# Kernel optimization log

Hardware: AMD Instinct MI355X
Metric: run time of the kernel (lower is better)

Reference implementation:

```python
import jax, jax.numpy as jnp
import numpy as np

NEG_INF = -1e30  # large negative in place of -inf for masked scores (fp32-safe)


def setup_inputs() -> dict:
    key = jax.random.key(0)
    kq, kk, kv, km = jax.random.split(key, 4)
    B, H, S, D = 2, 16, 2048, 64
    query = jax.random.normal(kq, (B, H, S, D), dtype=jnp.float32)
    k = jax.random.normal(kk, (B, H, S, D), dtype=jnp.float32)
    v = jax.random.normal(kv, (B, H, S, D), dtype=jnp.float32)
    mask = jax.random.randint(km, (B, H, S, S), 0, 2, dtype=jnp.int32)
    return {"query": query, "key": k, "value": v, "mask": mask}


def reference(query, key, value, mask):
    # Online-softmax chunked attention is mathematically exact softmax attention;
    # we compute the equivalent masked softmax attention in one fused expression.
    d_k = query.shape[-1]
    scale = 1.0 / np.sqrt(d_k).astype(np.float32)
    # scores: [B, H, Sq, Sk]
    scores = jnp.einsum('bhqd,bhkd->bhqk', query, key) * scale
    scores = jnp.where(mask == 0, NEG_INF, scores)
    attn = jax.nn.softmax(scores, axis=-1)
    out = jnp.einsum('bhqk,bhkd->bhqd', attn, value)
    return out
```

## Files before the change

kernel.cpp:

```cpp
#include <hip/hip_runtime.h>


typedef __attribute__((ext_vector_type(8))) short bf16x8;
typedef __attribute__((ext_vector_type(4))) short s16x4;
typedef __attribute__((ext_vector_type(4))) float f32x4;

#define S_LEN 2048
#define NT 32
#define PP 72
#define QSCALE 0.1803368801f

__device__ __forceinline__ short f2bf(float f) {
    union { float f; unsigned u; } v; v.f = f;
    unsigned r = v.u + 0x7fffu + ((v.u >> 16) & 1u);
    return (short)(r >> 16);
}

__device__ __forceinline__ float fexp2(float x) {
#if __has_builtin(__builtin_amdgcn_exp2f)
    return __builtin_amdgcn_exp2f(x);
#else
    return exp2f(x);
#endif
}

__device__ __forceinline__ bf16x8 cvt8(float4 a, float4 b, float s) {
    bf16x8 f;
    f[0]=f2bf(a.x*s); f[1]=f2bf(a.y*s); f[2]=f2bf(a.z*s); f[3]=f2bf(a.w*s);
    f[4]=f2bf(b.x*s); f[5]=f2bf(b.y*s); f[6]=f2bf(b.z*s); f[7]=f2bf(b.w*s);
    return f;
}

__global__ __launch_bounds__(256)
void pack_all(const float* __restrict__ Q, const float* __restrict__ K,
              const float* __restrict__ V, short* __restrict__ Qw,
              short* __restrict__ Kw, short* __restrict__ Vw) {
    __shared__ float vt[64][65];
    const int bh = blockIdx.x, t = blockIdx.y, which = blockIdx.z;
    if (which == 0) {
        for (int ci = threadIdx.x; ci < 512; ci += 256) {
            int ww = ci >> 7, ks = (ci >> 6) & 1, lane = ci & 63;
            int quad = lane >> 4, c = lane & 15;
            int row = t * 64 + ww * 16 + c;
            int d0 = ks * 32 + quad * 8;
            const float* src = Q + ((size_t)(bh * S_LEN + row)) * 64 + d0;
            float4 a = *(const float4*)src;
            float4 b = *(const float4*)(src + 4);
            *(bf16x8*)(Qw + ((size_t)(bh * 32 + t) * 512 + ci) * 8) = cvt8(a, b, QSCALE);
        }
    } else if (which == 1) {
        for (int ci = threadIdx.x; ci < 512; ci += 256) {
            int fb = ci >> 6, lane = ci & 63;
            int nb = fb >> 1, ks = fb & 1;
            int quad = lane >> 4, c = lane & 15;
            int key = t * 64 + c * 4 + nb;
            int d0 = ks * 32 + quad * 8;
            const float* src = K + ((size_t)(bh * S_LEN + key)) * 64 + d0;
            float4 a = *(const float4*)src;
            float4 b = *(const float4*)(src + 4);
            *(bf16x8*)(Kw + ((size_t)(bh * 32 + t) * 512 + ci) * 8) = cvt8(a, b, 1.0f);
        }
    } else {
        {
            int key = threadIdx.x >> 2, d0 = (threadIdx.x & 3) * 16;
            const float* src = V + ((size_t)(bh * S_LEN + t * 64 + key)) * 64 + d0;
            float4 a = *(const float4*)src;
            float4 b = *(const float4*)(src + 4);
            float4 cc = *(const float4*)(src + 8);
            float4 d = *(const float4*)(src + 12);
            float* dst = &vt[key][d0];
            dst[0]=a.x; dst[1]=a.y; dst[2]=a.z; dst[3]=a.w;
            dst[4]=b.x; dst[5]=b.y; dst[6]=b.z; dst[7]=b.w;
            dst[8]=cc.x; dst[9]=cc.y; dst[10]=cc.z; dst[11]=cc.w;
            dst[12]=d.x; dst[13]=d.y; dst[14]=d.z; dst[15]=d.w;
        }
        __syncthreads();
        for (int ci = threadIdx.x; ci < 512; ci += 256) {
            int fb = ci >> 6, lane = ci & 63;
            int db = fb >> 1, ks = fb & 1;
            int quad = lane >> 4, c = lane & 15;
            bf16x8 f;
#pragma unroll
            for (int j = 0; j < 8; ++j) {
                int pos = ks * 32 + quad * 8 + j;
                f[j] = f2bf(vt[pos][db * 16 + c]);
            }
            *(bf16x8*)(Vw + ((size_t)(bh * 32 + t) * 512 + ci) * 8) = f;
        }
    }
}

typedef __attribute__((address_space(3))) unsigned lds_u32;
typedef const __attribute__((address_space(1))) unsigned glob_u32;

__global__ __launch_bounds__(256, 3)
void fa_main(const short* __restrict__ Qw, const short* __restrict__ Kw,
             const short* __restrict__ Vw, const int* __restrict__ M,
             float* __restrict__ O) {
    __shared__ __align__(16) short Kb[2 * 8 * 512];
    __shared__ __align__(16) short Vb[2 * 8 * 512];
    __shared__ __align__(16) short Pwv[4 * 16 * PP];

    const int tid  = threadIdx.x;
    const int lane = tid & 63;
    const int w    = tid >> 6;
    const int quad = lane >> 4;
    const int c    = lane & 15;

    const int bid = blockIdx.x;
    const int x = bid & 7, y = bid >> 3;
    const int bh = x * 4 + (y >> 5);
    const int qt = y & 31;

    const short* qbase = Qw + ((size_t)(bh * 32 + qt) * 512 + w * 128 + lane) * 8;
    const bf16x8 qf0 = *(const bf16x8*)qbase;
    const bf16x8 qf1 = *(const bf16x8*)(qbase + 512);

    const bool isK = (w < 2);
    const short* gsrc = (isK ? Kw : Vw) + (size_t)bh * 32 * 4096 + (w & 1) * 2048 + (size_t)lane * 8;
    short* ldst0 = (isK ? Kb : Vb) + (w & 1) * 2048;

    const int* mrow = M + ((size_t)(bh * S_LEN + qt * 64 + w * 16 + quad * 4)) * S_LEN + 4 * c;

    f32x4 acco[4];
    float lacc[4];
#pragma unroll
    for (int r = 0; r < 4; ++r) {
        lacc[r] = 0.f;
        acco[r][0]=0.f; acco[r][1]=0.f; acco[r][2]=0.f; acco[r][3]=0.f;
    }

    if (isK) {
#pragma unroll
        for (int i = 0; i < 4; ++i)
            __builtin_amdgcn_global_load_lds((glob_u32*)(gsrc + i * 512),
                                             (lds_u32*)(ldst0 + i * 512), 16, 0, 0);
    }
    int4 mcur[4];
#pragma unroll
    for (int r = 0; r < 4; ++r) mcur[r] = *(const int4*)(mrow + (size_t)r * S_LEN);
    __syncthreads();

    short* pw = &Pwv[w * 16 * PP];
    const short* pr = &Pwv[w * 16 * PP + c * PP];

#pragma unroll 2
    for (int t = 0; t < NT; ++t) {
        const int tn = (t + 1) & (NT - 1);
        const int dtile = isK ? tn : t;
        const int dbuf = (dtile & 1) * 4096;
#pragma unroll
        for (int i = 0; i < 4; ++i)
            __builtin_amdgcn_global_load_lds((glob_u32*)(gsrc + (size_t)dtile * 4096 + i * 512),
                                             (lds_u32*)(ldst0 + dbuf + i * 512), 16, 0, 0);
        int4 mnxt[4];
#pragma unroll
        for (int r = 0; r < 4; ++r)
            mnxt[r] = *(const int4*)(mrow + (size_t)r * S_LEN + tn * 64);

        const int kc = (t & 1) * 4096;
        f32x4 accs[4];
#pragma unroll
        for (int nb = 0; nb < 4; ++nb) { accs[nb][0]=0.f; accs[nb][1]=0.f; accs[nb][2]=0.f; accs[nb][3]=0.f; }
#pragma unroll
        for (int nb = 0; nb < 4; ++nb) {
            bf16x8 b0 = *(const bf16x8*)&Kb[kc + (nb * 2 + 0) * 512 + lane * 8];
            accs[nb] = __builtin_amdgcn_mfma_f32_16x16x32_bf16(qf0, b0, accs[nb], 0, 0, 0);
            bf16x8 b1 = *(const bf16x8*)&Kb[kc + (nb * 2 + 1) * 512 + lane * 8];
            accs[nb] = __builtin_amdgcn_mfma_f32_16x16x32_bf16(qf1, b1, accs[nb], 0, 0, 0);
        }

        if (t > 0) {
            const int vc = ((t - 1) & 1) * 4096;
            bf16x8 pf0 = *(const bf16x8*)(pr + quad * 8);
            bf16x8 pf1 = *(const bf16x8*)(pr + 32 + quad * 8);
#pragma unroll
            for (int db = 0; db < 4; ++db) {
                bf16x8 v0 = *(const bf16x8*)&Vb[vc + (db * 2 + 0) * 512 + lane * 8];
                acco[db] = __builtin_amdgcn_mfma_f32_16x16x32_bf16(pf0, v0, acco[db], 0, 0, 0);
                bf16x8 v1 = *(const bf16x8*)&Vb[vc + (db * 2 + 1) * 512 + lane * 8];
                acco[db] = __builtin_amdgcn_mfma_f32_16x16x32_bf16(pf1, v1, acco[db], 0, 0, 0);
            }
        }

#pragma unroll
        for (int r = 0; r < 4; ++r) {
            const int4 mm = mcur[r];
            float e0 = fexp2(accs[0][r]); e0 = (mm.x != 0) ? e0 : 0.f;
            float e1 = fexp2(accs[1][r]); e1 = (mm.y != 0) ? e1 : 0.f;
            float e2 = fexp2(accs[2][r]); e2 = (mm.z != 0) ? e2 : 0.f;
            float e3 = fexp2(accs[3][r]); e3 = (mm.w != 0) ? e3 : 0.f;
            lacc[r] += (e0 + e1) + (e2 + e3);
            s16x4 pk = { f2bf(e0), f2bf(e1), f2bf(e2), f2bf(e3) };
            *(s16x4*)&pw[(quad * 4 + r) * PP + 4 * c] = pk;
        }
#pragma unroll
        for (int r = 0; r < 4; ++r) mcur[r] = mnxt[r];
        __syncthreads();
    }

    {
        const int vc = ((NT - 1) & 1) * 4096;
        bf16x8 pf0 = *(const bf16x8*)(pr + quad * 8);
        bf16x8 pf1 = *(const bf16x8*)(pr + 32 + quad * 8);
#pragma unroll
        for (int db = 0; db < 4; ++db) {
            bf16x8 v0 = *(const bf16x8*)&Vb[vc + (db * 2 + 0) * 512 + lane * 8];
            acco[db] = __builtin_amdgcn_mfma_f32_16x16x32_bf16(pf0, v0, acco[db], 0, 0, 0);
            bf16x8 v1 = *(const bf16x8*)&Vb[vc + (db * 2 + 1) * 512 + lane * 8];
            acco[db] = __builtin_amdgcn_mfma_f32_16x16x32_bf16(pf1, v1, acco[db], 0, 0, 0);
        }
    }

    float* orow = O + ((size_t)(bh * S_LEN + qt * 64 + w * 16 + quad * 4)) * 64 + c;
#pragma unroll
    for (int r = 0; r < 4; ++r) {
        float l = lacc[r];
        l += __shfl_xor(l, 1);
        l += __shfl_xor(l, 2);
        l += __shfl_xor(l, 4);
        l += __shfl_xor(l, 8);
        float inv = 1.0f / l;
#pragma unroll
        for (int db = 0; db < 4; ++db)
            orow[(size_t)r * 64 + db * 16] = acco[db][r] * inv;
    }
}

extern "C" void kernel_launch(void* const* d_in, const int* in_sizes, int n_in,
                              void* d_out, int out_size, void* d_ws, size_t ws_size,
                              hipStream_t stream) {
    const float* Q = (const float*)d_in[0];
    const float* K = (const float*)d_in[1];
    const float* V = (const float*)d_in[2];
    const int*   M = (const int*)d_in[3];
    float* O = (float*)d_out;

    short* Qw = (short*)d_ws;
    short* Kw = Qw + (size_t)32 * 32 * 4096;
    short* Vw = Kw + (size_t)32 * 32 * 4096;

    hipLaunchKernelGGL(pack_all, dim3(32, 32, 3), dim3(256), 0, stream, Q, K, V, Qw, Kw, Vw);
    hipLaunchKernelGGL(fa_main, dim3(1024), dim3(256), 0, stream, Qw, Kw, Vw, M, O);
}
```

Before: 748.8 us.

## Process two query tiles per block to reuse K/V tiles across both

Each block now handles 128 query rows (two 64-row subtiles) instead of 64, so every K/V tile loaded into LDS feeds twice the MFMA work and the grid is halved to 512 blocks. It also switches bf16 packing of probabilities to a hardware packed-convert builtin where available. The cost is double the accumulator and mask registers per thread, launch bounds lowered to 2 waves-per-EU occupancy, fewer blocks to fill the GPU, and the unroll-2 hint is removed. The kernel is mostly bound by streaming the int32 mask, which is unchanged.

```diff
diff --git a/kernel.cpp b/kernel.cpp
--- a/kernel.cpp
+++ b/kernel.cpp
@@ -23,6 +23,18 @@
     return exp2f(x);
 #endif
 }
+
+#if __has_builtin(__builtin_amdgcn_cvt_pk_bf16_f32)
+typedef __attribute__((ext_vector_type(2))) __bf16 bf16x2_t;
+__device__ __forceinline__ unsigned pk2(float a, float b) {
+    bf16x2_t v = __builtin_amdgcn_cvt_pk_bf16_f32(a, b);
+    union { bf16x2_t v; unsigned u; } u; u.v = v; return u.u;
+}
+#else
+__device__ __forceinline__ unsigned pk2(float a, float b) {
+    return (unsigned)(unsigned short)f2bf(a) | ((unsigned)(unsigned short)f2bf(b) << 16);
+}
+#endif
 
 __device__ __forceinline__ bf16x8 cvt8(float4 a, float4 b, float s) {
     bf16x8 f;
@@ -93,13 +105,15 @@
 typedef __attribute__((address_space(3))) unsigned lds_u32;
 typedef const __attribute__((address_space(1))) unsigned glob_u32;
 
-__global__ __launch_bounds__(256, 3)
+#define MFMA(a, b, acc) __builtin_amdgcn_mfma_f32_16x16x32_bf16(a, b, acc, 0, 0, 0)
+
+__global__ __launch_bounds__(256, 2)
 void fa_main(const short* __restrict__ Qw, const short* __restrict__ Kw,
              const short* __restrict__ Vw, const int* __restrict__ M,
              float* __restrict__ O) {
     __shared__ __align__(16) short Kb[2 * 8 * 512];
     __shared__ __align__(16) short Vb[2 * 8 * 512];
-    __shared__ __align__(16) short Pwv[4 * 16 * PP];
+    __shared__ __align__(16) short Pwv[8 * 16 * PP];
 
     const int tid  = threadIdx.x;
     const int lane = tid & 63;
@@ -109,26 +123,34 @@
 
     const int bid = blockIdx.x;
     const int x = bid & 7, y = bid >> 3;
-    const int bh = x * 4 + (y >> 5);
-    const int qt = y & 31;
-
-    const short* qbase = Qw + ((size_t)(bh * 32 + qt) * 512 + w * 128 + lane) * 8;
-    const bf16x8 qf0 = *(const bf16x8*)qbase;
-    const bf16x8 qf1 = *(const bf16x8*)(qbase + 512);
+    const int bh = x * 4 + (y >> 4);
+    const int p  = y & 15;
+
+    bf16x8 qf[2][2];
+#pragma unroll
+    for (int s = 0; s < 2; ++s) {
+        const short* qb = Qw + ((size_t)(bh * 32 + 2 * p + s) * 512 + w * 128 + lane) * 8;
+        qf[s][0] = *(const bf16x8*)qb;
+        qf[s][1] = *(const bf16x8*)(qb + 512);
+    }
 
     const bool isK = (w < 2);
     const short* gsrc = (isK ? Kw : Vw) + (size_t)bh * 32 * 4096 + (w & 1) * 2048 + (size_t)lane * 8;
     short* ldst0 = (isK ? Kb : Vb) + (w & 1) * 2048;
 
-    const int* mrow = M + ((size_t)(bh * S_LEN + qt * 64 + w * 16 + quad * 4)) * S_LEN + 4 * c;
-
-    f32x4 acco[4];
-    float lacc[4];
-#pragma unroll
-    for (int r = 0; r < 4; ++r) {
-        lacc[r] = 0.f;
-        acco[r][0]=0.f; acco[r][1]=0.f; acco[r][2]=0.f; acco[r][3]=0.f;
-    }
+    const int* mrow[2];
+    mrow[0] = M + ((size_t)(bh * S_LEN + p * 128 + w * 16 + quad * 4)) * S_LEN + 4 * c;
+    mrow[1] = mrow[0] + (size_t)64 * S_LEN;
+
+    f32x4 acco[2][4];
+    float lacc[2][4];
+#pragma unroll
+    for (int s = 0; s < 2; ++s)
+#pragma unroll
+        for (int r = 0; r < 4; ++r) {
+            lacc[s][r] = 0.f;
+            acco[s][r][0]=0.f; acco[s][r][1]=0.f; acco[s][r][2]=0.f; acco[s][r][3]=0.f;
+        }
 
     if (isK) {
 #pragma unroll
@@ -136,15 +158,20 @@
             __builtin_amdgcn_global_load_lds((glob_u32*)(gsrc + i * 512),
                                              (lds_u32*)(ldst0 + i * 512), 16, 0, 0);
     }
-    int4 mcur[4];
-#pragma unroll
-    for (int r = 0; r < 4; ++r) mcur[r] = *(const int4*)(mrow + (size_t)r * S_LEN);
+    int4 mcur[2][4];
+#pragma unroll
+    for (int s = 0; s < 2; ++s)
+#pragma unroll
+        for (int r = 0; r < 4; ++r)
+            mcur[s][r] = *(const int4*)(mrow[s] + (size_t)r * S_LEN);
     __syncthreads();
 
-    short* pw = &Pwv[w * 16 * PP];
-    const short* pr = &Pwv[w * 16 * PP + c * PP];
-
-#pragma unroll 2
+    short* pw[2];
+    pw[0] = &Pwv[(0 + w) * 16 * PP];
+    pw[1] = &Pwv[(4 + w) * 16 * PP];
+    const short* pr0 = pw[0] + c * PP;
+    const short* pr1 = pw[1] + c * PP;
+
     for (int t = 0; t < NT; ++t) {
         const int tn = (t + 1) & (NT - 1);
         const int dtile = isK ? tn : t;
@@ -153,77 +180,102 @@
         for (int i = 0; i < 4; ++i)
             __builtin_amdgcn_global_load_lds((glob_u32*)(gsrc + (size_t)dtile * 4096 + i * 512),
                                              (lds_u32*)(ldst0 + dbuf + i * 512), 16, 0, 0);
-        int4 mnxt[4];
-#pragma unroll
-        for (int r = 0; r < 4; ++r)
-            mnxt[r] = *(const int4*)(mrow + (size_t)r * S_LEN + tn * 64);
+        int4 mnxt[2][4];
+#pragma unroll
+        for (int s = 0; s < 2; ++s)
+#pragma unroll
+            for (int r = 0; r < 4; ++r)
+                mnxt[s][r] = *(const int4*)(mrow[s] + (size_t)r * S_LEN + tn * 64);
 
         const int kc = (t & 1) * 4096;
-        f32x4 accs[4];
-#pragma unroll
-        for (int nb = 0; nb < 4; ++nb) { accs[nb][0]=0.f; accs[nb][1]=0.f; accs[nb][2]=0.f; accs[nb][3]=0.f; }
+        f32x4 accs[2][4];
+#pragma unroll
+        for (int s = 0; s < 2; ++s)
+#pragma unroll
+            for (int nb = 0; nb < 4; ++nb) { accs[s][nb][0]=0.f; accs[s][nb][1]=0.f; accs[s][nb][2]=0.f; accs[s][nb][3]=0.f; }
 #pragma unroll
         for (int nb = 0; nb < 4; ++nb) {
             bf16x8 b0 = *(const bf16x8*)&Kb[kc + (nb * 2 + 0) * 512 + lane * 8];
-            accs[nb] = __builtin_amdgcn_mfma_f32_16x16x32_bf16(qf0, b0, accs[nb], 0, 0, 0);
             bf16x8 b1 = *(const bf16x8*)&Kb[kc + (nb * 2 + 1) * 512 + lane * 8];
-            accs[nb] = __builtin_amdgcn_mfma_f32_16x16x32_bf16(qf1, b1, accs[nb], 0, 0, 0);
+            accs[0][nb] = MFMA(qf[0][0], b0, accs[0][nb]);
+            accs[0][nb] = MFMA(qf[0][1], b1, accs[0][nb]);
+            accs[1][nb] = MFMA(qf[1][0], b0, accs[1][nb]);
+            accs[1][nb] = MFMA(qf[1][1], b1, accs[1][nb]);
         }
 
         if (t > 0) {
             const int vc = ((t - 1) & 1) * 4096;
-            bf16x8 pf0 = *(const bf16x8*)(pr + quad * 8);
-            bf16x8 pf1 = *(const bf16x8*)(pr + 32 + quad * 8);
+            bf16x8 pf00 = *(const bf16x8*)(pr0 + quad * 8);
+            bf16x8 pf01 = *(const bf16x8*)(pr0 + 32 + quad * 8);
+            bf16x8 pf10 = *(const bf16x8*)(pr1 + quad * 8);
+            bf16x8 pf11 = *(const bf16x8*)(pr1 + 32 + quad * 8);
 #pragma unroll
             for (int db = 0; db < 4; ++db) {
                 bf16x8 v0 = *(const bf16x8*)&Vb[vc + (db * 2 + 0) * 512 + lane * 8];
-                acco[db] = __builtin_amdgcn_mfma_f32_16x16x32_bf16(pf0, v0, acco[db], 0, 0, 0);
                 bf16x8 v1 = *(const bf16x8*)&Vb[vc + (db * 2 + 1) * 512 + lane * 8];
-                acco[db] = __builtin_amdgcn_mfma_f32_16x16x32_bf16(pf1, v1, acco[db], 0, 0, 0);
+                acco[0][db] = MFMA(pf00, v0, acco[0][db]);
+                acco[0][db] = MFMA(pf01, v1, acco[0][db]);
+                acco[1][db] = MFMA(pf10, v0, acco[1][db]);
+                acco[1][db] = MFMA(pf11, v1, acco[1][db]);
             }
         }
 
 #pragma unroll
-        for (int r = 0; r < 4; ++r) {
-            const int4 mm = mcur[r];
-            float e0 = fexp2(accs[0][r]); e0 = (mm.x != 0) ? e0 : 0.f;
-            float e1 = fexp2(accs[1][r]); e1 = (mm.y != 0) ? e1 : 0.f;
-            float e2 = fexp2(accs[2][r]); e2 = (mm.z != 0) ? e2 : 0.f;
-            float e3 = fexp2(accs[3][r]); e3 = (mm.w != 0) ? e3 : 0.f;
-            lacc[r] += (e0 + e1) + (e2 + e3);
-            s16x4 pk = { f2bf(e0), f2bf(e1), f2bf(e2), f2bf(e3) };
-            *(s16x4*)&pw[(quad * 4 + r) * PP + 4 * c] = pk;
-        }
-#pragma unroll
-        for (int r = 0; r < 4; ++r) mcur[r] = mnxt[r];
+        for (int s = 0; s < 2; ++s) {
+            short* pws = pw[s];
+#pragma unroll
+            for (int r = 0; r < 4; ++r) {
+                const int4 mm = mcur[s][r];
+                float e0 = fexp2(accs[s][0][r]); e0 = (mm.x != 0) ? e0 : 0.f;
+                float e1 = fexp2(accs[s][1][r]); e1 = (mm.y != 0) ? e1 : 0.f;
+                float e2 = fexp2(accs[s][2][r]); e2 = (mm.z != 0) ? e2 : 0.f;
+                float e3 = fexp2(accs[s][3][r]); e3 = (mm.w != 0) ? e3 : 0.f;
+                lacc[s][r] += (e0 + e1) + (e2 + e3);
+                union { unsigned u[2]; s16x4 v; } pk;
+                pk.u[0] = pk2(e0, e1);
+                pk.u[1] = pk2(e2, e3);
+                *(s16x4*)&pws[(quad * 4 + r) * PP + 4 * c] = pk.v;
+            }
+        }
+#pragma unroll
+        for (int s = 0; s < 2; ++s)
+#pragma unroll
+            for (int r = 0; r < 4; ++r) mcur[s][r] = mnxt[s][r];
         __syncthreads();
     }
 
     {
         const int vc = ((NT - 1) & 1) * 4096;
-        bf16x8 pf0 = *(const bf16x8*)(pr + quad * 8);
-        bf16x8 pf1 = *(const bf16x8*)(pr + 32 + quad * 8);
+        bf16x8 pf00 = *(const bf16x8*)(pr0 + quad * 8);
+        bf16x8 pf01 = *(const bf16x8*)(pr0 + 32 + quad * 8);
+        bf16x8 pf10 = *(const bf16x8*)(pr1 + quad * 8);
+        bf16x8 pf11 = *(const bf16x8*)(pr1 + 32 + quad * 8);
 #pragma unroll
         for (int db = 0; db < 4; ++db) {
             bf16x8 v0 = *(const bf16x8*)&Vb[vc + (db * 2 + 0) * 512 + lane * 8];
-            acco[db] = __builtin_amdgcn_mfma_f32_16x16x32_bf16(pf0, v0, acco[db], 0, 0, 0);
             bf16x8 v1 = *(const bf16x8*)&Vb[vc + (db * 2 + 1) * 512 + lane * 8];
-            acco[db] = __builtin_amdgcn_mfma_f32_16x16x32_bf16(pf1, v1, acco[db], 0, 0, 0);
-        }
-    }
-
-    float* orow = O + ((size_t)(bh * S_LEN + qt * 64 + w * 16 + quad * 4)) * 64 + c;
-#pragma unroll
-    for (int r = 0; r < 4; ++r) {
-        float l = lacc[r];
-        l += __shfl_xor(l, 1);
-        l += __shfl_xor(l, 2);
-        l += __shfl_xor(l, 4);
-        l += __shfl_xor(l, 8);
-        float inv = 1.0f / l;
-#pragma unroll
-        for (int db = 0; db < 4; ++db)
-            orow[(size_t)r * 64 + db * 16] = acco[db][r] * inv;
+            acco[0][db] = MFMA(pf00, v0, acco[0][db]);
+            acco[0][db] = MFMA(pf01, v1, acco[0][db]);
+            acco[1][db] = MFMA(pf10, v0, acco[1][db]);
+            acco[1][db] = MFMA(pf11, v1, acco[1][db]);
+        }
+    }
+
+#pragma unroll
+    for (int s = 0; s < 2; ++s) {
+        float* orow = O + ((size_t)(bh * S_LEN + p * 128 + s * 64 + w * 16 + quad * 4)) * 64 + c;
+#pragma unroll
+        for (int r = 0; r < 4; ++r) {
+            float l = lacc[s][r];
+            l += __shfl_xor(l, 1);
+            l += __shfl_xor(l, 2);
+            l += __shfl_xor(l, 4);
+            l += __shfl_xor(l, 8);
+            float inv = 1.0f / l;
+#pragma unroll
+            for (int db = 0; db < 4; ++db)
+                orow[(size_t)r * 64 + db * 16] = acco[s][db][r] * inv;
+        }
     }
 }
 
@@ -241,5 +293,5 @@
     short* Vw = Kw + (size_t)32 * 32 * 4096;
 
     hipLaunchKernelGGL(pack_all, dim3(32, 32, 3), dim3(256), 0, stream, Q, K, V, Qw, Kw, Vw);
-    hipLaunchKernelGGL(fa_main, dim3(1024), dim3(256), 0, stream, Qw, Kw, Vw, M, O);
-}
+    hipLaunchKernelGGL(fa_main, dim3(512), dim3(256), 0, stream, Qw, Kw, Vw, M, O);
+}
```

Result: no change. 752.7 us (+0.5%).
